# Kernel optimization log

Measured on AMD Instinct MI355X. Metric: run time of the kernel, lower is better.

The kernel has to match this reference:

```python
import jax, jax.numpy as jnp
import numpy as np
from jax.ops import segment_sum

N, E, D, H = 50000, 800000, 128, 128


def setup_inputs() -> dict:
    key = jax.random.key(0)
    ks = jax.random.split(key, 8)
    x = jax.random.normal(ks[0], (N, D), dtype=jnp.float32)
    edge_index = jax.random.randint(ks[1], (2, E), 0, N, dtype=jnp.int64)
    # Glorot-ish scaled weights for 3 GCNConv layers
    s0 = 1.0 / np.sqrt(D)
    s1 = 1.0 / np.sqrt(H)
    W0 = jax.random.normal(ks[2], (D, H), dtype=jnp.float32) * s0
    W1 = jax.random.normal(ks[3], (H, H), dtype=jnp.float32) * s1
    W2 = jax.random.normal(ks[4], (H, H), dtype=jnp.float32) * s1
    b0 = jnp.zeros((H,), dtype=jnp.float32)
    b1 = jnp.zeros((H,), dtype=jnp.float32)
    b2 = jnp.zeros((H,), dtype=jnp.float32)
    return {"x": x, "edge_index": edge_index,
            "W0": W0, "b0": b0, "W1": W1, "b1": b1, "W2": W2, "b2": b2}


def _gcn_norm(edge_index, num_nodes):
    # Add self-loops, compute symmetric normalization deg^-1/2 A deg^-1/2
    loops = jnp.arange(num_nodes, dtype=edge_index.dtype)
    src = jnp.concatenate([edge_index[0], loops])  # [E+N]
    dst = jnp.concatenate([edge_index[1], loops])  # [E+N]
    deg = segment_sum(jnp.ones_like(dst, dtype=jnp.float32), dst,
                      num_segments=num_nodes)       # in-degree incl. self-loop
    dinv = jnp.where(deg > 0, jax.lax.rsqrt(deg), 0.0)
    norm = dinv[src] * dinv[dst]                    # [E+N]
    return src, dst, norm


def _gcn_conv(x, src, dst, norm, W, b, num_nodes):
    h = x @ W                                        # [N, H] linear first (PyG order)
    msg = h[src] * norm[:, None]                     # gather + scale
    agg = segment_sum(msg, dst, num_segments=num_nodes)  # scatter-add
    return agg + b


def reference(x, edge_index, W0, b0, W1, b1, W2, b2):
    num_nodes = x.shape[0]
    src, dst, norm = _gcn_norm(edge_index, num_nodes)
    for W, b in ((W0, b0), (W1, b1), (W2, b2)):
        x = jax.nn.relu(_gcn_conv(x, src, dst, norm, W, b, num_nodes))
    return x
```

## Files before the change

### kernel.cpp

```cpp
#include <hip/hip_runtime.h>


typedef __attribute__((ext_vector_type(8))) unsigned short ushort8;
typedef __attribute__((ext_vector_type(8))) short short8v;
typedef __attribute__((ext_vector_type(4))) float f32x4;

#define BCAP 64

__device__ __forceinline__ unsigned short f2bf(float f) {
    unsigned u = __float_as_uint(f);
    unsigned r = (u + 0x7FFF + ((u >> 16) & 1)) >> 16;
    return (unsigned short)r;
}
__device__ __forceinline__ float bf2f(unsigned short s) {
    return __uint_as_float(((unsigned)s) << 16);
}

__global__ __launch_bounds__(256) void prep0_kernel(int4* __restrict__ cntv, int n4, int zblk,
                                                    const float* __restrict__ W0,
                                                    const float* __restrict__ W1,
                                                    const float* __restrict__ W2,
                                                    short* __restrict__ F0,
                                                    short* __restrict__ F1,
                                                    short* __restrict__ F2) {
    int bid = blockIdx.x;
    if (bid < zblk) {
        int i = bid * 256 + threadIdx.x;
        if (i < n4) cntv[i] = make_int4(0, 0, 0, 0);
        return;
    }
    int wb = bid - zblk;
    int which = wb >> 3;
    const float* W = which == 0 ? W0 : (which == 1 ? W1 : W2);
    short* Wfrag   = which == 0 ? F0 : (which == 1 ? F1 : F2);
    int idx = (wb & 7) * 256 + threadIdx.x;
    int l = idx & 63;
    int cks = idx >> 6;
    int ks = cks & 3, c = cks >> 2;
    int col = c * 16 + (l & 15);
    int k0 = ks * 32 + (l >> 4) * 8;
    short8v o;
#pragma unroll
    for (int j = 0; j < 8; ++j) o[j] = (short)f2bf(W[(size_t)(k0 + j) * 128 + col]);
    ((short8v*)Wfrag)[idx] = o;
}

template <bool IN_BF16, bool SCALE>
__device__ __forceinline__ void gemm_body(int bid, const void* __restrict__ Xv,
                                          const short* __restrict__ Wfrag,
                                          const int* __restrict__ cnt,
                                          unsigned short* __restrict__ G, int n) {
    int t = threadIdx.x;
    int wv = t >> 6, l = t & 63;
    int row0 = bid * 64 + wv * 16;
    int r = l & 15, half = l >> 4;
    int arow = row0 + r;
    bool rok = arow < n;

    f32x4 acc[8];
#pragma unroll
    for (int c = 0; c < 8; ++c) acc[c] = (f32x4){0.f, 0.f, 0.f, 0.f};

    const short8v* WF = (const short8v*)Wfrag;

#pragma unroll
    for (int ks = 0; ks < 4; ++ks) {
        short8v a = (short8v){0, 0, 0, 0, 0, 0, 0, 0};
        if (rok) {
            if (IN_BF16) {
                const unsigned short* X = (const unsigned short*)Xv;
                a = *(const short8v*)(X + (size_t)arow * 128 + ks * 32 + half * 8);
            } else {
                const float* X = (const float*)Xv;
                const float4* xp = (const float4*)(X + (size_t)arow * 128 + ks * 32 + half * 8);
                float4 x0 = xp[0], x1 = xp[1];
                a[0] = (short)f2bf(x0.x); a[1] = (short)f2bf(x0.y);
                a[2] = (short)f2bf(x0.z); a[3] = (short)f2bf(x0.w);
                a[4] = (short)f2bf(x1.x); a[5] = (short)f2bf(x1.y);
                a[6] = (short)f2bf(x1.z); a[7] = (short)f2bf(x1.w);
            }
        }
#pragma unroll
        for (int c = 0; c < 8; ++c) {
            short8v b = WF[(c * 4 + ks) * 64 + l];
            acc[c] = __builtin_amdgcn_mfma_f32_16x16x32_bf16(a, b, acc[c], 0, 0, 0);
        }
    }

    float ds[4];
    int orow[4];
#pragma unroll
    for (int i = 0; i < 4; ++i) {
        orow[i] = row0 + half * 4 + i;
        ds[i] = 1.f;
        if (SCALE)
            ds[i] = (orow[i] < n) ? rsqrtf((float)(cnt[orow[i]] + 1)) : 0.f;
    }
#pragma unroll
    for (int c = 0; c < 8; ++c) {
#pragma unroll
        for (int i = 0; i < 4; ++i) {
            if (orow[i] < n)
                G[(size_t)orow[i] * 128 + c * 16 + r] = f2bf(ds[i] * acc[c][i]);
        }
    }
}

__global__ __launch_bounds__(256) void cg_kernel(const float* __restrict__ X,
                                                 const short* __restrict__ Wfrag,
                                                 unsigned short* __restrict__ H, int n, int gblk,
                                                 const int* __restrict__ ei,
                                                 int* __restrict__ cnt,
                                                 unsigned short* __restrict__ col, int E) {
    int bid = blockIdx.x;
    if (bid < gblk) {
        gemm_body<false, false>(bid, X, Wfrag, nullptr, H, n);
        return;
    }
    int e = ((bid - gblk) * 256 + threadIdx.x) * 4;
    if (e + 4 <= E) {
        int4 s4 = *(const int4*)(ei + e);
        int4 d4 = *(const int4*)(ei + E + e);
        int r0 = atomicAdd(&cnt[d4.x], 1);
        int r1 = atomicAdd(&cnt[d4.y], 1);
        int r2 = atomicAdd(&cnt[d4.z], 1);
        int r3 = atomicAdd(&cnt[d4.w], 1);
        if (r0 < BCAP) col[(size_t)d4.x * BCAP + r0] = (unsigned short)s4.x;
        if (r1 < BCAP) col[(size_t)d4.y * BCAP + r1] = (unsigned short)s4.y;
        if (r2 < BCAP) col[(size_t)d4.z * BCAP + r2] = (unsigned short)s4.z;
        if (r3 < BCAP) col[(size_t)d4.w * BCAP + r3] = (unsigned short)s4.w;
    } else {
        for (; e < E; ++e) {
            int d = ei[E + e];
            int r = atomicAdd(&cnt[d], 1);
            if (r < BCAP) col[(size_t)d * BCAP + r] = (unsigned short)ei[e];
        }
    }
}

__global__ __launch_bounds__(256) void gemm_mfma_kernel(const void* __restrict__ Xv,
                                                        const short* __restrict__ Wfrag,
                                                        const int* __restrict__ cnt,
                                                        unsigned short* __restrict__ G, int n) {
    gemm_body<true, true>(blockIdx.x, Xv, Wfrag, cnt, G, n);
}

__global__ __launch_bounds__(256) void scale_kernel(const unsigned short* __restrict__ H,
                                                    const int* __restrict__ cnt,
                                                    unsigned short* __restrict__ G, int n) {
    int idx = blockIdx.x * 256 + threadIdx.x;
    int row = idx >> 4, q = idx & 15;
    if (row < n) {
        float d = rsqrtf((float)(cnt[row] + 1));
        ushort8 h = *(const ushort8*)(H + (size_t)row * 128 + q * 8);
        ushort8 o;
#pragma unroll
        for (int j = 0; j < 8; ++j) o[j] = f2bf(d * bf2f(h[j]));
        *(ushort8*)(G + (size_t)row * 128 + q * 8) = o;
    }
}

template <bool OUT_BF16>
__global__ __launch_bounds__(256) void agg_kernel(const unsigned short* __restrict__ G,
                                                  const int* __restrict__ cnt,
                                                  const unsigned short* __restrict__ col,
                                                  const float* __restrict__ b,
                                                  void* __restrict__ outv, int n) {
    int gw = (int)((blockIdx.x * blockDim.x + threadIdx.x) >> 6);
    if (gw >= n) return;
    int lane = threadIdx.x & 63;
    int q = lane & 15, p = lane >> 4;
    int deg = cnt[gw];
    if (deg > BCAP) deg = BCAP;
    int beg = gw * BCAP, end = beg + deg;
    float di = rsqrtf((float)(deg + 1));

    ushort8 gs = *(const ushort8*)(G + (size_t)gw * 128 + q * 8);

    float acc[8];
#pragma unroll
    for (int j = 0; j < 8; ++j) acc[j] = 0.f;

    int nit = (deg + 7) >> 3;

    auto issue = [&](int s, ushort8& h0, ushort8& h1, float& m0, float& m1) {
        int i0 = beg + s * 8 + p;
        int i1 = i0 + 4;
        bool v0 = i0 < end, v1 = i1 < end;
        int c0 = col[v0 ? i0 : beg];
        int c1 = col[v1 ? i1 : beg];
        m0 = v0 ? 1.f : 0.f;
        m1 = v1 ? 1.f : 0.f;
        h0 = *(const ushort8*)(G + (size_t)c0 * 128 + q * 8);
        h1 = *(const ushort8*)(G + (size_t)c1 * 128 + q * 8);
    };

    ushort8 h0a = {}, h1a = {}, h0b = {}, h1b = {};
    float m0a = 0.f, m1a = 0.f, m0b = 0.f, m1b = 0.f;

    if (nit > 0) issue(0, h0a, h1a, m0a, m1a);
    if (nit > 1) issue(1, h0b, h1b, m0b, m1b);
    for (int s = 0; s < nit; ++s) {
#pragma unroll
        for (int j = 0; j < 8; ++j) {
            acc[j] = fmaf(m0a, bf2f(h0a[j]), acc[j]);
            acc[j] = fmaf(m1a, bf2f(h1a[j]), acc[j]);
        }
        h0a = h0b; h1a = h1b; m0a = m0b; m1a = m1b;
        if (s + 2 < nit) issue(s + 2, h0b, h1b, m0b, m1b);
    }

#pragma unroll
    for (int j = 0; j < 8; ++j) {
        acc[j] += __shfl_xor(acc[j], 16);
        acc[j] += __shfl_xor(acc[j], 32);
    }

    if (p == 0) {
        float4 b0 = *(const float4*)(b + q * 8);
        float4 b1 = *(const float4*)(b + q * 8 + 4);
        float o[8];
#pragma unroll
        for (int j = 0; j < 8; ++j) o[j] = di * (acc[j] + bf2f(gs[j]));
        o[0] += b0.x; o[1] += b0.y; o[2] += b0.z; o[3] += b0.w;
        o[4] += b1.x; o[5] += b1.y; o[6] += b1.z; o[7] += b1.w;
#pragma unroll
        for (int j = 0; j < 8; ++j) o[j] = fmaxf(o[j], 0.f);
        if (OUT_BF16) {
            ushort8 ov;
#pragma unroll
            for (int j = 0; j < 8; ++j) ov[j] = f2bf(o[j]);
            *(ushort8*)((unsigned short*)outv + (size_t)gw * 128 + q * 8) = ov;
        } else {
            float* out = (float*)outv;
            *(float4*)(out + (size_t)gw * 128 + q * 8)     = make_float4(o[0], o[1], o[2], o[3]);
            *(float4*)(out + (size_t)gw * 128 + q * 8 + 4) = make_float4(o[4], o[5], o[6], o[7]);
        }
    }
}

extern "C" void kernel_launch(void* const* d_in, const int* in_sizes, int n_in,
                              void* d_out, int out_size, void* d_ws, size_t ws_size,
                              hipStream_t stream) {
    const float* x  = (const float*)d_in[0];
    const int*   ei = (const int*)d_in[1];
    const float* W0 = (const float*)d_in[2];
    const float* b0 = (const float*)d_in[3];
    const float* W1 = (const float*)d_in[4];
    const float* b1 = (const float*)d_in[5];
    const float* W2 = (const float*)d_in[6];
    const float* b2 = (const float*)d_in[7];
    float* out = (float*)d_out;

    int N = in_sizes[0] / 128;
    int E = in_sizes[1] / 2;

    char* wsb = (char*)d_ws;
    size_t off = 0;
    auto alloc = [&](size_t bytes) -> void* {
        void* p = wsb + off;
        off = (off + bytes + 255) & ~(size_t)255;
        return p;
    };
    int*            cnt = (int*)           alloc((size_t)N * 4);
    unsigned short* col = (unsigned short*)alloc((size_t)N * BCAP * 2);
    unsigned short* g   = (unsigned short*)alloc((size_t)N * 128 * 2);
    unsigned short* h   = (unsigned short*)alloc((size_t)N * 128 * 2);
    unsigned short* xB  = (unsigned short*)alloc((size_t)N * 128 * 2);
    short* wf0    = (short*)alloc(128 * 128 * 2);
    short* wf1    = (short*)alloc(128 * 128 * 2);
    short* wf2    = (short*)alloc(128 * 128 * 2);

    int n4 = (N + 3) / 4;
    int zblk = (n4 + 255) / 256;
    int gblk = (N + 63) / 64;
    int e4 = (E + 3) / 4;
    int cblk = (e4 + 255) / 256;
    int sblk = (N * 16 + 255) / 256;
    int ablk = (N + 3) / 4;

    prep0_kernel<<<zblk + 24, 256, 0, stream>>>((int4*)cnt, n4, zblk,
                                                W0, W1, W2, wf0, wf1, wf2);
    cg_kernel<<<gblk + cblk, 256, 0, stream>>>(x, wf0, h, N, gblk, ei, cnt, col, E);
    scale_kernel<<<sblk, 256, 0, stream>>>(h, cnt, g, N);

    agg_kernel<true><<<ablk, 256, 0, stream>>>(g, cnt, col, b0, xB, N);

    gemm_mfma_kernel<<<gblk, 256, 0, stream>>>(xB, wf1, cnt, g, N);
    agg_kernel<true><<<ablk, 256, 0, stream>>>(g, cnt, col, b1, xB, N);

    gemm_mfma_kernel<<<gblk, 256, 0, stream>>>(xB, wf2, cnt, g, N);
    agg_kernel<false><<<ablk, 256, 0, stream>>>(g, cnt, col, b2, out, N);
}
```

Measured before the change: 189.3 us.

## Partition edge bucketing by destination range across eight block groups

The CSR-like bucketing of edges by destination is reorganized so each of eight partition groups reads every edge chunk but only performs atomics and column writes for destinations in its node range. This is meant to localize atomic and scattered-write traffic into a smaller address window per block, improving cache/L2 locality. The cost is reading the edge list eight times and extra filtering work.

```diff
diff --git a/kernel.cpp b/kernel.cpp
--- a/kernel.cpp
+++ b/kernel.cpp
@@ -6,6 +6,7 @@
 typedef __attribute__((ext_vector_type(4))) float f32x4;
 
 #define BCAP 64
+#define CHUNK 4096
 
 __device__ __forceinline__ unsigned short f2bf(float f) {
     unsigned u = __float_as_uint(f);
@@ -117,23 +118,45 @@
         gemm_body<false, false>(bid, X, Wfrag, nullptr, H, n);
         return;
     }
-    int e = ((bid - gblk) * 256 + threadIdx.x) * 4;
-    if (e + 4 <= E) {
-        int4 s4 = *(const int4*)(ei + e);
-        int4 d4 = *(const int4*)(ei + E + e);
-        int r0 = atomicAdd(&cnt[d4.x], 1);
-        int r1 = atomicAdd(&cnt[d4.y], 1);
-        int r2 = atomicAdd(&cnt[d4.z], 1);
-        int r3 = atomicAdd(&cnt[d4.w], 1);
-        if (r0 < BCAP) col[(size_t)d4.x * BCAP + r0] = (unsigned short)s4.x;
-        if (r1 < BCAP) col[(size_t)d4.y * BCAP + r1] = (unsigned short)s4.y;
-        if (r2 < BCAP) col[(size_t)d4.z * BCAP + r2] = (unsigned short)s4.z;
-        if (r3 < BCAP) col[(size_t)d4.w * BCAP + r3] = (unsigned short)s4.w;
-    } else {
-        for (; e < E; ++e) {
-            int d = ei[E + e];
-            int r = atomicAdd(&cnt[d], 1);
-            if (r < BCAP) col[(size_t)d * BCAP + r] = (unsigned short)ei[e];
+    int pid = bid - gblk;
+    int part = pid & 7;
+    int sub = pid >> 3;
+    int PS = (n + 7) >> 3;
+    int lo = part * PS;
+    int hi = lo + PS; if (hi > n) hi = n;
+    int base = sub * CHUNK;
+    int t = threadIdx.x;
+
+#pragma unroll
+    for (int i = 0; i < CHUNK / 1024; ++i) {
+        int e = base + i * 1024 + t * 4;
+        if (e + 4 <= E) {
+            int4 d4 = *(const int4*)(ei + E + e);
+            int4 s4 = *(const int4*)(ei + e);
+            if (d4.x >= lo && d4.x < hi) {
+                int r = atomicAdd(&cnt[d4.x], 1);
+                if (r < BCAP) col[(size_t)d4.x * BCAP + r] = (unsigned short)s4.x;
+            }
+            if (d4.y >= lo && d4.y < hi) {
+                int r = atomicAdd(&cnt[d4.y], 1);
+                if (r < BCAP) col[(size_t)d4.y * BCAP + r] = (unsigned short)s4.y;
+            }
+            if (d4.z >= lo && d4.z < hi) {
+                int r = atomicAdd(&cnt[d4.z], 1);
+                if (r < BCAP) col[(size_t)d4.z * BCAP + r] = (unsigned short)s4.z;
+            }
+            if (d4.w >= lo && d4.w < hi) {
+                int r = atomicAdd(&cnt[d4.w], 1);
+                if (r < BCAP) col[(size_t)d4.w * BCAP + r] = (unsigned short)s4.w;
+            }
+        } else {
+            for (; e < E; ++e) {
+                int d = ei[E + e];
+                if (d >= lo && d < hi) {
+                    int r = atomicAdd(&cnt[d], 1);
+                    if (r < BCAP) col[(size_t)d * BCAP + r] = (unsigned short)ei[e];
+                }
+            }
         }
     }
 }
@@ -274,8 +297,8 @@
     int n4 = (N + 3) / 4;
     int zblk = (n4 + 255) / 256;
     int gblk = (N + 63) / 64;
-    int e4 = (E + 3) / 4;
-    int cblk = (e4 + 255) / 256;
+    int nsub = (E + CHUNK - 1) / CHUNK;
+    int cblk = 8 * nsub;
     int sblk = (N * 16 + 255) / 256;
     int ablk = (N + 3) / 4;
 
```

After: 188.5 us. No clear change (-0.4%).
